# Kernel tuning notes

Measured on AMD Instinct MI355X. Metric: run time of the kernel, lower is better.

## Reference

```python
import jax, jax.numpy as jnp
import numpy as np

EPS = 1e-10
NUM_NODES = 100000
OUT_CH = 128
NUM_EDGES = 600000


def setup_inputs() -> dict:
    key = jax.random.key(0)
    k1, k2, k3, k4, k5, k6 = jax.random.split(key, 6)
    emb = jax.random.normal(k1, (NUM_NODES, OUT_CH), dtype=jnp.float32) * 0.02
    edge_index = jax.random.randint(k2, (2, NUM_EDGES), 0, NUM_NODES, dtype=jnp.int32)
    edge_norm = jax.random.uniform(k3, (NUM_EDGES,), dtype=jnp.float32)
    lim = 1.0 / np.sqrt(OUT_CH)
    loc_w = jax.random.uniform(k4, (OUT_CH, OUT_CH), minval=-lim, maxval=lim, dtype=jnp.float32)
    loc_b = jnp.zeros((OUT_CH,), dtype=jnp.float32)
    std_w = jax.random.uniform(k5, (OUT_CH, OUT_CH), minval=-lim, maxval=lim, dtype=jnp.float32)
    std_b = jnp.zeros((OUT_CH,), dtype=jnp.float32)
    return {"emb": emb, "loc_w": loc_w, "loc_b": loc_b, "std_w": std_w,
            "std_b": std_b, "edge_index": edge_index, "edge_norm": edge_norm}


def reference(emb, loc_w, loc_b, std_w, std_b, edge_index, edge_norm):
    sidx, tidx = edge_index[0], edge_index[1]
    # gather-scale-scatter graph conv: message[e] = emb[sidx[e]] * enorm[e]
    message = emb[sidx] * edge_norm[:, None]          # [E, C]
    ptr = jax.ops.segment_sum(message, tidx, num_segments=emb.shape[0])  # [N, C]
    loc = ptr @ loc_w.T + loc_b                        # [N, C]
    std = jax.nn.softplus(ptr @ std_w.T + std_b) + EPS # [N, C]
    # eval mode: emb_out = loc (dist is Normal(loc, std), returned as params)
    return (loc, std)
```

## Files before the change

### kernel.cpp

```cpp
#include <hip/hip_runtime.h>
#include <hip/hip_bf16.h>
#include <stdint.h>

#define OUT_CH 128
#define EPSV 1e-10f

typedef __attribute__((ext_vector_type(4))) float f32x4;
typedef __attribute__((ext_vector_type(8))) short bf16x8;

__device__ __forceinline__ ushort f2bf(float f) {
    union { float f; unsigned u; } a; a.f = f;
    unsigned u = a.u;
    unsigned r = (u + 0x7fffu + ((u >> 16) & 1u)) >> 16;
    return (ushort)r;
}

__global__ __launch_bounds__(256) void hist_convert_kernel(
    const int* __restrict__ eidx, int* __restrict__ cnt, int E, int HB, int EB,
    const float* __restrict__ locw, const float* __restrict__ stdw,
    int4* __restrict__ Wb, const float* __restrict__ emb, int4* __restrict__ embb4)
{
    int b = blockIdx.x;
    if (b < HB) {
        int e = b * 256 + threadIdx.x;
        if (e < E) atomicAdd(&cnt[eidx[E + e]], 1);
    } else if (b < HB + 16) {
        int q = (b - HB) * 256 + threadIdx.x;
        int r = q >> 4;
        int c = q & 15;
        const float* src = (r < 128) ? (locw + r * 128 + c * 8)
                                     : (stdw + (r - 128) * 128 + c * 8);
        float4 u0 = *reinterpret_cast<const float4*>(src);
        float4 u1 = *reinterpret_cast<const float4*>(src + 4);
        unsigned p0 = (unsigned)f2bf(u0.x) | ((unsigned)f2bf(u0.y) << 16);
        unsigned p1 = (unsigned)f2bf(u0.z) | ((unsigned)f2bf(u0.w) << 16);
        unsigned p2 = (unsigned)f2bf(u1.x) | ((unsigned)f2bf(u1.y) << 16);
        unsigned p3 = (unsigned)f2bf(u1.z) | ((unsigned)f2bf(u1.w) << 16);
        Wb[q] = make_int4((int)p0, (int)p1, (int)p2, (int)p3);
    } else {
        int idx8 = (b - HB - 16) * 256 + threadIdx.x;
        const float4* e4 = (const float4*)emb;
        float4 u0 = e4[(size_t)idx8 * 2];
        float4 u1 = e4[(size_t)idx8 * 2 + 1];
        unsigned p0 = (unsigned)f2bf(u0.x) | ((unsigned)f2bf(u0.y) << 16);
        unsigned p1 = (unsigned)f2bf(u0.z) | ((unsigned)f2bf(u0.w) << 16);
        unsigned p2 = (unsigned)f2bf(u1.x) | ((unsigned)f2bf(u1.y) << 16);
        unsigned p3 = (unsigned)f2bf(u1.z) | ((unsigned)f2bf(u1.w) << 16);
        embb4[idx8] = make_int4((int)p0, (int)p1, (int)p2, (int)p3);
    }
}

__device__ __forceinline__ int block_exscan256(int v, int* lds, int* totalOut) {
    int t = threadIdx.x;
    lds[t] = v; __syncthreads();
    #pragma unroll
    for (int d = 1; d < 256; d <<= 1) {
        int x = (t >= d) ? lds[t - d] : 0;
        __syncthreads();
        lds[t] += x;
        __syncthreads();
    }
    int inc = lds[t];
    int tot = lds[255];
    __syncthreads();
    *totalOut = tot;
    return inc - v;
}

__global__ __launch_bounds__(256) void block_sum_kernel(
    const int* __restrict__ cnt, int* __restrict__ bsum, int N)
{
    __shared__ int lds[256];
    int base = blockIdx.x * 1024;
    int local = 0;
    #pragma unroll
    for (int k = 0; k < 4; ++k) {
        int idx = base + threadIdx.x * 4 + k;
        local += (idx < N) ? cnt[idx] : 0;
    }
    lds[threadIdx.x] = local; __syncthreads();
    for (int d = 128; d > 0; d >>= 1) {
        if (threadIdx.x < d) lds[threadIdx.x] += lds[threadIdx.x + d];
        __syncthreads();
    }
    if (threadIdx.x == 0) bsum[blockIdx.x] = lds[0];
}

__global__ __launch_bounds__(256) void top_scan_kernel(
    const int* __restrict__ bsum, int* __restrict__ bofs, int NB)
{
    __shared__ int lds[256];
    int t = threadIdx.x;
    int v = (t < NB) ? bsum[t] : 0;
    int total;
    int ex = block_exscan256(v, lds, &total);
    if (t < NB) bofs[t] = ex;
}

__global__ __launch_bounds__(256) void scan_final_kernel(
    const int* __restrict__ cnt, const int* __restrict__ bofs,
    int* __restrict__ cursor, int N)
{
    __shared__ int lds[256];
    int base = blockIdx.x * 1024;
    int c[4]; int local = 0;
    #pragma unroll
    for (int k = 0; k < 4; ++k) {
        int idx = base + threadIdx.x * 4 + k;
        c[k] = (idx < N) ? cnt[idx] : 0;
        local += c[k];
    }
    int total;
    int ex = block_exscan256(local, lds, &total);
    int run = bofs[blockIdx.x] + ex;
    #pragma unroll
    for (int k = 0; k < 4; ++k) {
        int idx = base + threadIdx.x * 4 + k;
        if (idx < N) { cursor[idx] = run; run += c[k]; }
    }
}

__global__ __launch_bounds__(256) void fill_kernel(
    const int* __restrict__ eidx, const float* __restrict__ enorm,
    int* __restrict__ cursor, int2* __restrict__ srcw, int E)
{
    int e = blockIdx.x * 256 + threadIdx.x;
    if (e >= E) return;
    int t = eidx[E + e];
    int s = eidx[e];
    float w = enorm[e];
    int pos = atomicAdd(&cursor[t], 1);
    srcw[pos] = make_int2(s, __float_as_int(w));
}

__global__ __launch_bounds__(256) void gather_kernel(
    const unsigned* __restrict__ embb, const int* __restrict__ cursor,
    const int* __restrict__ cnt, const int2* __restrict__ srcw,
    unsigned* __restrict__ ptrb, int N)
{
    int wid = (blockIdx.x * 256 + threadIdx.x) >> 6;
    if (wid >= N) return;
    int lane = threadIdx.x & 63;
    int c = cnt[wid];
    int o = cursor[wid] - c;
    float ax = 0.f, ay = 0.f;
    int j = 0;
    for (; j + 4 <= c; j += 4) {
        int2 p0 = srcw[o + j + 0];
        int2 p1 = srcw[o + j + 1];
        int2 p2 = srcw[o + j + 2];
        int2 p3 = srcw[o + j + 3];
        unsigned v0 = embb[(size_t)p0.x * 64 + lane];
        unsigned v1 = embb[(size_t)p1.x * 64 + lane];
        unsigned v2 = embb[(size_t)p2.x * 64 + lane];
        unsigned v3 = embb[(size_t)p3.x * 64 + lane];
        float w0 = __int_as_float(p0.y), w1 = __int_as_float(p1.y);
        float w2 = __int_as_float(p2.y), w3 = __int_as_float(p3.y);
        ax += __uint_as_float(v0 << 16) * w0 + __uint_as_float(v1 << 16) * w1
            + __uint_as_float(v2 << 16) * w2 + __uint_as_float(v3 << 16) * w3;
        ay += __uint_as_float(v0 & 0xffff0000u) * w0 + __uint_as_float(v1 & 0xffff0000u) * w1
            + __uint_as_float(v2 & 0xffff0000u) * w2 + __uint_as_float(v3 & 0xffff0000u) * w3;
    }
    for (; j < c; ++j) {
        int2 p = srcw[o + j];
        float w = __int_as_float(p.y);
        unsigned v = embb[(size_t)p.x * 64 + lane];
        ax += __uint_as_float(v << 16) * w;
        ay += __uint_as_float(v & 0xffff0000u) * w;
    }
    ptrb[(size_t)wid * 128 + lane] = (unsigned)f2bf(ax) | ((unsigned)f2bf(ay) << 16);
}

__global__ __launch_bounds__(256, 4) void gemm_kernel(
    const int4* __restrict__ Wb, const float* __restrict__ locb,
    const float* __restrict__ stdb, float* __restrict__ out, int N)
{
    __shared__ ushort Wt[128 * 128];
    const int t = threadIdx.x;
    const int wave = t >> 6;
    const int lane = t & 63;
    const int grp = lane >> 4;
    const int l16 = lane & 15;
    const int base = blockIdx.x * 128 + wave * 32;

    const ushort* ptrb = (const ushort*)out;
    int r0 = base + l16;      if (r0 > N - 1) r0 = N - 1;
    int r1 = base + 16 + l16; if (r1 > N - 1) r1 = N - 1;

    bf16x8 a0[4], a1[4];
    #pragma unroll
    for (int s = 0; s < 4; ++s) {
        a0[s] = *reinterpret_cast<const bf16x8*>(ptrb + (size_t)r0 * 256 + s * 32 + grp * 8);
        a1[s] = *reinterpret_cast<const bf16x8*>(ptrb + (size_t)r1 * 256 + s * 32 + grp * 8);
    }

    #pragma unroll
    for (int h = 0; h < 2; ++h) {
        if (h) __syncthreads();
        #pragma unroll
        for (int i = 0; i < 8; ++i) {
            int q = i * 256 + t;
            int r = q >> 4;
            int c = q & 15;
            *reinterpret_cast<int4*>(&Wt[r * 128 + ((c ^ (r & 15)) << 3)]) =
                Wb[(h * 128 + r) * 16 + c];
        }
        __syncthreads();

        f32x4 acc0[8], acc1[8];
        #pragma unroll
        for (int j = 0; j < 8; ++j) {
            acc0[j] = (f32x4){0.f, 0.f, 0.f, 0.f};
            acc1[j] = (f32x4){0.f, 0.f, 0.f, 0.f};
        }

        #pragma unroll
        for (int j = 0; j < 8; ++j) {
            int cb = (j * 16 + l16) * 128;
            #pragma unroll
            for (int s = 0; s < 4; ++s) {
                int c = s * 4 + grp;
                bf16x8 bfr = *reinterpret_cast<const bf16x8*>(&Wt[cb + ((c ^ l16) << 3)]);
                acc0[j] = __builtin_amdgcn_mfma_f32_16x16x32_bf16(a0[s], bfr, acc0[j], 0, 0, 0);
                acc1[j] = __builtin_amdgcn_mfma_f32_16x16x32_bf16(a1[s], bfr, acc1[j], 0, 0, 0);
            }
        }

        float* dst = h ? (out + (size_t)N * OUT_CH) : out;
        #pragma unroll
        for (int j = 0; j < 8; ++j) {
            int col = j * 16 + l16;
            float bias = h ? stdb[col] : locb[col];
            #pragma unroll
            for (int tile = 0; tile < 2; ++tile) {
                #pragma unroll
                for (int rg = 0; rg < 4; ++rg) {
                    int node = base + tile * 16 + grp * 4 + rg;
                    if (node < N) {
                        float x = (tile ? acc1[j][rg] : acc0[j][rg]) + bias;
                        if (h) x = __logf(1.0f + __expf(x)) + EPSV;
                        dst[(size_t)node * OUT_CH + col] = x;
                    }
                }
            }
        }
    }
}

extern "C" void kernel_launch(void* const* d_in, const int* in_sizes, int n_in,
                              void* d_out, int out_size, void* d_ws, size_t ws_size,
                              hipStream_t stream) {
    const float* emb  = (const float*)d_in[0];
    const float* locw = (const float*)d_in[1];
    const float* locb = (const float*)d_in[2];
    const float* stdw = (const float*)d_in[3];
    const float* stdb = (const float*)d_in[4];
    const int*   eidx = (const int*)d_in[5];
    const float* enorm= (const float*)d_in[6];
    float* out = (float*)d_out;

    const int N = in_sizes[0] / OUT_CH;
    const int E = in_sizes[6];
    const int NB = (N + 1023) / 1024;
    const int HB = (E + 255) / 256;
    const int EB = (N * (OUT_CH / 8) + 255) / 256;

    int* cnt    = (int*)d_ws;
    int* cursor = cnt + N;
    int* bsum   = cursor + N;
    int* bofs   = bsum + 256;
    int2* srcw  = (int2*)(((uintptr_t)(bofs + 256) + 255) & ~(uintptr_t)255);
    int4* Wb    = (int4*)(((uintptr_t)(srcw + E) + 255) & ~(uintptr_t)255);

    unsigned* embb = (unsigned*)(out + (size_t)N * OUT_CH);

    hipMemsetAsync(cnt, 0, (size_t)N * sizeof(int), stream);

    hist_convert_kernel<<<HB + 16 + EB, 256, 0, stream>>>(
        eidx, cnt, E, HB, EB, locw, stdw, Wb, emb, (int4*)embb);
    block_sum_kernel<<<NB, 256, 0, stream>>>(cnt, bsum, N);
    top_scan_kernel<<<1, 256, 0, stream>>>(bsum, bofs, NB);
    scan_final_kernel<<<NB, 256, 0, stream>>>(cnt, bofs, cursor, N);
    fill_kernel<<<(E + 255) / 256, 256, 0, stream>>>(eidx, enorm, cursor, srcw, E);

    unsigned* ptrb = (unsigned*)out;
    long gthreads = (long)N * 64;
    gather_kernel<<<(int)((gthreads + 255) / 256), 256, 0, stream>>>(embb, cursor, cnt, srcw, ptrb, N);

    int nblocks = (N + 127) / 128;
    gemm_kernel<<<nblocks, 256, 0, stream>>>(Wb, locb, stdb, out, N);
}
```

Before: 293.0 us.

## Merge three-pass scan into one kernel and gather two nodes per wave

Replaces the three-kernel prefix scan (block sums, top scan, final scan) with a single 1024-thread block in which each thread serially scans a contiguous chunk of counts. This removes two launches and their inter-kernel gaps. The gather kernel now gives each node 32 lanes that each load 8 bytes (four bf16 channels), so one 64-lane wave handles two nodes and issues wider loads. The trade-off is that the single-block scan runs on one CU and each thread walks about 98 elements serially with uncoalesced strided reads.

Result: slower. 428.2 us (+46.2%).

```diff
diff --git a/kernel.cpp b/kernel.cpp
--- a/kernel.cpp
+++ b/kernel.cpp
@@ -14,6 +14,9 @@
     unsigned r = (u + 0x7fffu + ((u >> 16) & 1u)) >> 16;
     return (ushort)r;
 }
+
+__device__ __forceinline__ float bflo(unsigned u) { return __uint_as_float(u << 16); }
+__device__ __forceinline__ float bfhi(unsigned u) { return __uint_as_float(u & 0xffff0000u); }
 
 __global__ __launch_bounds__(256) void hist_convert_kernel(
     const int* __restrict__ eidx, int* __restrict__ cnt, int E, int HB, int EB,
@@ -50,74 +53,26 @@
     }
 }
 
-__device__ __forceinline__ int block_exscan256(int v, int* lds, int* totalOut) {
+__global__ __launch_bounds__(1024) void scan_kernel(
+    const int* __restrict__ cnt, int* __restrict__ cursor, int N)
+{
+    __shared__ int lds[1024];
     int t = threadIdx.x;
-    lds[t] = v; __syncthreads();
+    int CH = (N + 1023) >> 10;
+    int s = t * CH;
+    int e = s + CH; if (e > N) e = N;
+    int local = 0;
+    for (int i = s; i < e; ++i) local += cnt[i];
+    lds[t] = local; __syncthreads();
     #pragma unroll
-    for (int d = 1; d < 256; d <<= 1) {
+    for (int d = 1; d < 1024; d <<= 1) {
         int x = (t >= d) ? lds[t - d] : 0;
         __syncthreads();
         lds[t] += x;
         __syncthreads();
     }
-    int inc = lds[t];
-    int tot = lds[255];
-    __syncthreads();
-    *totalOut = tot;
-    return inc - v;
-}
-
-__global__ __launch_bounds__(256) void block_sum_kernel(
-    const int* __restrict__ cnt, int* __restrict__ bsum, int N)
-{
-    __shared__ int lds[256];
-    int base = blockIdx.x * 1024;
-    int local = 0;
-    #pragma unroll
-    for (int k = 0; k < 4; ++k) {
-        int idx = base + threadIdx.x * 4 + k;
-        local += (idx < N) ? cnt[idx] : 0;
-    }
-    lds[threadIdx.x] = local; __syncthreads();
-    for (int d = 128; d > 0; d >>= 1) {
-        if (threadIdx.x < d) lds[threadIdx.x] += lds[threadIdx.x + d];
-        __syncthreads();
-    }
-    if (threadIdx.x == 0) bsum[blockIdx.x] = lds[0];
-}
-
-__global__ __launch_bounds__(256) void top_scan_kernel(
-    const int* __restrict__ bsum, int* __restrict__ bofs, int NB)
-{
-    __shared__ int lds[256];
-    int t = threadIdx.x;
-    int v = (t < NB) ? bsum[t] : 0;
-    int total;
-    int ex = block_exscan256(v, lds, &total);
-    if (t < NB) bofs[t] = ex;
-}
-
-__global__ __launch_bounds__(256) void scan_final_kernel(
-    const int* __restrict__ cnt, const int* __restrict__ bofs,
-    int* __restrict__ cursor, int N)
-{
-    __shared__ int lds[256];
-    int base = blockIdx.x * 1024;
-    int c[4]; int local = 0;
-    #pragma unroll
-    for (int k = 0; k < 4; ++k) {
-        int idx = base + threadIdx.x * 4 + k;
-        c[k] = (idx < N) ? cnt[idx] : 0;
-        local += c[k];
-    }
-    int total;
-    int ex = block_exscan256(local, lds, &total);
-    int run = bofs[blockIdx.x] + ex;
-    #pragma unroll
-    for (int k = 0; k < 4; ++k) {
-        int idx = base + threadIdx.x * 4 + k;
-        if (idx < N) { cursor[idx] = run; run += c[k]; }
-    }
+    int run = lds[t] - local;
+    for (int i = s; i < e; ++i) { cursor[i] = run; run += cnt[i]; }
 }
 
 __global__ __launch_bounds__(256) void fill_kernel(
@@ -134,41 +89,46 @@
 }
 
 __global__ __launch_bounds__(256) void gather_kernel(
-    const unsigned* __restrict__ embb, const int* __restrict__ cursor,
+    const uint2* __restrict__ embb2, const int* __restrict__ cursor,
     const int* __restrict__ cnt, const int2* __restrict__ srcw,
-    unsigned* __restrict__ ptrb, int N)
-{
-    int wid = (blockIdx.x * 256 + threadIdx.x) >> 6;
-    if (wid >= N) return;
-    int lane = threadIdx.x & 63;
-    int c = cnt[wid];
-    int o = cursor[wid] - c;
-    float ax = 0.f, ay = 0.f;
+    uint2* __restrict__ ptrb2, int N)
+{
+    int h = (blockIdx.x * 256 + threadIdx.x) >> 5;
+    if (h >= N) return;
+    int lane = threadIdx.x & 31;
+    int c = cnt[h];
+    int o = cursor[h] - c;
+    float a0 = 0.f, a1 = 0.f, a2 = 0.f, a3 = 0.f;
     int j = 0;
     for (; j + 4 <= c; j += 4) {
         int2 p0 = srcw[o + j + 0];
         int2 p1 = srcw[o + j + 1];
         int2 p2 = srcw[o + j + 2];
         int2 p3 = srcw[o + j + 3];
-        unsigned v0 = embb[(size_t)p0.x * 64 + lane];
-        unsigned v1 = embb[(size_t)p1.x * 64 + lane];
-        unsigned v2 = embb[(size_t)p2.x * 64 + lane];
-        unsigned v3 = embb[(size_t)p3.x * 64 + lane];
+        uint2 v0 = embb2[(size_t)p0.x * 32 + lane];
+        uint2 v1 = embb2[(size_t)p1.x * 32 + lane];
+        uint2 v2 = embb2[(size_t)p2.x * 32 + lane];
+        uint2 v3 = embb2[(size_t)p3.x * 32 + lane];
         float w0 = __int_as_float(p0.y), w1 = __int_as_float(p1.y);
         float w2 = __int_as_float(p2.y), w3 = __int_as_float(p3.y);
-        ax += __uint_as_float(v0 << 16) * w0 + __uint_as_float(v1 << 16) * w1
-            + __uint_as_float(v2 << 16) * w2 + __uint_as_float(v3 << 16) * w3;
-        ay += __uint_as_float(v0 & 0xffff0000u) * w0 + __uint_as_float(v1 & 0xffff0000u) * w1
-            + __uint_as_float(v2 & 0xffff0000u) * w2 + __uint_as_float(v3 & 0xffff0000u) * w3;
+        a0 += bflo(v0.x) * w0 + bflo(v1.x) * w1 + bflo(v2.x) * w2 + bflo(v3.x) * w3;
+        a1 += bfhi(v0.x) * w0 + bfhi(v1.x) * w1 + bfhi(v2.x) * w2 + bfhi(v3.x) * w3;
+        a2 += bflo(v0.y) * w0 + bflo(v1.y) * w1 + bflo(v2.y) * w2 + bflo(v3.y) * w3;
+        a3 += bfhi(v0.y) * w0 + bfhi(v1.y) * w1 + bfhi(v2.y) * w2 + bfhi(v3.y) * w3;
     }
     for (; j < c; ++j) {
         int2 p = srcw[o + j];
         float w = __int_as_float(p.y);
-        unsigned v = embb[(size_t)p.x * 64 + lane];
-        ax += __uint_as_float(v << 16) * w;
-        ay += __uint_as_float(v & 0xffff0000u) * w;
-    }
-    ptrb[(size_t)wid * 128 + lane] = (unsigned)f2bf(ax) | ((unsigned)f2bf(ay) << 16);
+        uint2 v = embb2[(size_t)p.x * 32 + lane];
+        a0 += bflo(v.x) * w;
+        a1 += bfhi(v.x) * w;
+        a2 += bflo(v.y) * w;
+        a3 += bfhi(v.y) * w;
+    }
+    uint2 r;
+    r.x = (unsigned)f2bf(a0) | ((unsigned)f2bf(a1) << 16);
+    r.y = (unsigned)f2bf(a2) | ((unsigned)f2bf(a3) << 16);
+    ptrb2[(size_t)h * 64 + lane] = r;
 }
 
 __global__ __launch_bounds__(256, 4) void gemm_kernel(
@@ -261,15 +221,12 @@
 
     const int N = in_sizes[0] / OUT_CH;
     const int E = in_sizes[6];
-    const int NB = (N + 1023) / 1024;
     const int HB = (E + 255) / 256;
     const int EB = (N * (OUT_CH / 8) + 255) / 256;
 
     int* cnt    = (int*)d_ws;
     int* cursor = cnt + N;
-    int* bsum   = cursor + N;
-    int* bofs   = bsum + 256;
-    int2* srcw  = (int2*)(((uintptr_t)(bofs + 256) + 255) & ~(uintptr_t)255);
+    int2* srcw  = (int2*)(((uintptr_t)(cursor + N) + 255) & ~(uintptr_t)255);
     int4* Wb    = (int4*)(((uintptr_t)(srcw + E) + 255) & ~(uintptr_t)255);
 
     unsigned* embb = (unsigned*)(out + (size_t)N * OUT_CH);
@@ -278,14 +235,13 @@
 
     hist_convert_kernel<<<HB + 16 + EB, 256, 0, stream>>>(
         eidx, cnt, E, HB, EB, locw, stdw, Wb, emb, (int4*)embb);
-    block_sum_kernel<<<NB, 256, 0, stream>>>(cnt, bsum, N);
-    top_scan_kernel<<<1, 256, 0, stream>>>(bsum, bofs, NB);
-    scan_final_kernel<<<NB, 256, 0, stream>>>(cnt, bofs, cursor, N);
+    scan_kernel<<<1, 1024, 0, stream>>>(cnt, cursor, N);
     fill_kernel<<<(E + 255) / 256, 256, 0, stream>>>(eidx, enorm, cursor, srcw, E);
 
-    unsigned* ptrb = (unsigned*)out;
-    long gthreads = (long)N * 64;
-    gather_kernel<<<(int)((gthreads + 255) / 256), 256, 0, stream>>>(embb, cursor, cnt, srcw, ptrb, N);
+    uint2* ptrb2 = (uint2*)out;
+    long gthreads = (long)N * 32;
+    gather_kernel<<<(int)((gthreads + 255) / 256), 256, 0, stream>>>(
+        (const uint2*)embb, cursor, cnt, srcw, ptrb2, N);
 
     int nblocks = (N + 127) / 128;
     gemm_kernel<<<nblocks, 256, 0, stream>>>(Wb, locb, stdb, out, N);
```

## Gather with 16 lanes per node using 128-bit bf16 loads

Applied to the files above, without the earlier changes.

The gather kernel now gives each destination node 16 lanes instead of a full 64-lane wave. Each lane loads a uint4 holding 8 bf16 values and keeps 8 accumulators, so one wave processes four nodes at once. The goal is to cut wasted wave slots and the per-edge srcw load overhead, and to use wider memory transactions. The cost is more registers per lane, a shallower unroll (2 edges instead of 4), and more divergence between nodes with different degrees inside a wave. The output store stride is kept at 32 uint4 per row so the bf16 layout the GEMM reads from the fp32 buffer is unchanged.

After: 279.8 us. -4.5%, faster.

```diff
diff --git a/kernel.cpp b/kernel.cpp
--- a/kernel.cpp
+++ b/kernel.cpp
@@ -14,6 +14,9 @@
     unsigned r = (u + 0x7fffu + ((u >> 16) & 1u)) >> 16;
     return (ushort)r;
 }
+
+__device__ __forceinline__ float bflo(unsigned u) { return __uint_as_float(u << 16); }
+__device__ __forceinline__ float bfhi(unsigned u) { return __uint_as_float(u & 0xffff0000u); }
 
 __global__ __launch_bounds__(256) void hist_convert_kernel(
     const int* __restrict__ eidx, int* __restrict__ cnt, int E, int HB, int EB,
@@ -134,41 +137,48 @@
 }
 
 __global__ __launch_bounds__(256) void gather_kernel(
-    const unsigned* __restrict__ embb, const int* __restrict__ cursor,
+    const uint4* __restrict__ embb4, const int* __restrict__ cursor,
     const int* __restrict__ cnt, const int2* __restrict__ srcw,
-    unsigned* __restrict__ ptrb, int N)
-{
-    int wid = (blockIdx.x * 256 + threadIdx.x) >> 6;
-    if (wid >= N) return;
-    int lane = threadIdx.x & 63;
-    int c = cnt[wid];
-    int o = cursor[wid] - c;
-    float ax = 0.f, ay = 0.f;
+    uint4* __restrict__ ptrb4, int N)
+{
+    int q = (blockIdx.x * 256 + threadIdx.x) >> 4;
+    if (q >= N) return;
+    int l16 = threadIdx.x & 15;
+    int c = cnt[q];
+    int o = cursor[q] - c;
+    float a0 = 0.f, a1 = 0.f, a2 = 0.f, a3 = 0.f;
+    float a4 = 0.f, a5 = 0.f, a6 = 0.f, a7 = 0.f;
     int j = 0;
-    for (; j + 4 <= c; j += 4) {
+    for (; j + 2 <= c; j += 2) {
         int2 p0 = srcw[o + j + 0];
         int2 p1 = srcw[o + j + 1];
-        int2 p2 = srcw[o + j + 2];
-        int2 p3 = srcw[o + j + 3];
-        unsigned v0 = embb[(size_t)p0.x * 64 + lane];
-        unsigned v1 = embb[(size_t)p1.x * 64 + lane];
-        unsigned v2 = embb[(size_t)p2.x * 64 + lane];
-        unsigned v3 = embb[(size_t)p3.x * 64 + lane];
+        uint4 v0 = embb4[(size_t)p0.x * 16 + l16];
+        uint4 v1 = embb4[(size_t)p1.x * 16 + l16];
         float w0 = __int_as_float(p0.y), w1 = __int_as_float(p1.y);
-        float w2 = __int_as_float(p2.y), w3 = __int_as_float(p3.y);
-        ax += __uint_as_float(v0 << 16) * w0 + __uint_as_float(v1 << 16) * w1
-            + __uint_as_float(v2 << 16) * w2 + __uint_as_float(v3 << 16) * w3;
-        ay += __uint_as_float(v0 & 0xffff0000u) * w0 + __uint_as_float(v1 & 0xffff0000u) * w1
-            + __uint_as_float(v2 & 0xffff0000u) * w2 + __uint_as_float(v3 & 0xffff0000u) * w3;
-    }
-    for (; j < c; ++j) {
+        a0 += bflo(v0.x) * w0 + bflo(v1.x) * w1;
+        a1 += bfhi(v0.x) * w0 + bfhi(v1.x) * w1;
+        a2 += bflo(v0.y) * w0 + bflo(v1.y) * w1;
+        a3 += bfhi(v0.y) * w0 + bfhi(v1.y) * w1;
+        a4 += bflo(v0.z) * w0 + bflo(v1.z) * w1;
+        a5 += bfhi(v0.z) * w0 + bfhi(v1.z) * w1;
+        a6 += bflo(v0.w) * w0 + bflo(v1.w) * w1;
+        a7 += bfhi(v0.w) * w0 + bfhi(v1.w) * w1;
+    }
+    if (j < c) {
         int2 p = srcw[o + j];
+        uint4 v = embb4[(size_t)p.x * 16 + l16];
         float w = __int_as_float(p.y);
-        unsigned v = embb[(size_t)p.x * 64 + lane];
-        ax += __uint_as_float(v << 16) * w;
-        ay += __uint_as_float(v & 0xffff0000u) * w;
-    }
-    ptrb[(size_t)wid * 128 + lane] = (unsigned)f2bf(ax) | ((unsigned)f2bf(ay) << 16);
+        a0 += bflo(v.x) * w;  a1 += bfhi(v.x) * w;
+        a2 += bflo(v.y) * w;  a3 += bfhi(v.y) * w;
+        a4 += bflo(v.z) * w;  a5 += bfhi(v.z) * w;
+        a6 += bflo(v.w) * w;  a7 += bfhi(v.w) * w;
+    }
+    uint4 r;
+    r.x = (unsigned)f2bf(a0) | ((unsigned)f2bf(a1) << 16);
+    r.y = (unsigned)f2bf(a2) | ((unsigned)f2bf(a3) << 16);
+    r.z = (unsigned)f2bf(a4) | ((unsigned)f2bf(a5) << 16);
+    r.w = (unsigned)f2bf(a6) | ((unsigned)f2bf(a7) << 16);
+    ptrb4[(size_t)q * 32 + l16] = r;
 }
 
 __global__ __launch_bounds__(256, 4) void gemm_kernel(
@@ -283,9 +293,10 @@
     scan_final_kernel<<<NB, 256, 0, stream>>>(cnt, bofs, cursor, N);
     fill_kernel<<<(E + 255) / 256, 256, 0, stream>>>(eidx, enorm, cursor, srcw, E);
 
-    unsigned* ptrb = (unsigned*)out;
-    long gthreads = (long)N * 64;
-    gather_kernel<<<(int)((gthreads + 255) / 256), 256, 0, stream>>>(embb, cursor, cnt, srcw, ptrb, N);
+    uint4* ptrb4 = (uint4*)out;
+    long gthreads = (long)N * 16;
+    gather_kernel<<<(int)((gthreads + 255) / 256), 256, 0, stream>>>(
+        (const uint4*)embb, cursor, cnt, srcw, ptrb4, N);
 
     int nblocks = (N + 127) / 128;
     gemm_kernel<<<nblocks, 256, 0, stream>>>(Wb, locb, stdb, out, N);
```
